# Kernel tuning notes

Hardware: AMD Instinct MI355X
Metric: run time of the kernel (lower is better)

The kernel has to match this reference:

```python
import jax, jax.numpy as jnp
import numpy as np


def setup_inputs() -> dict:
    key = jax.random.key(0)
    k1, k2 = jax.random.split(key)
    T, D, E = 8192, 4096, 64
    x = jax.random.normal(k1, (T, D), dtype=jnp.float32)
    gate_w = jax.random.normal(k2, (E, D), dtype=jnp.float32) * (1.0 / np.sqrt(D))
    return {"x": x, "gate_w": gate_w}


def reference(x, gate_w):
    TOPK = 8
    # logits = x @ W^T, computed in float32 like .float() in torch
    logits = jnp.einsum('td,ed->te', x, gate_w).astype(jnp.float32)
    scores = jax.nn.sigmoid(scores_in := logits) if False else jax.nn.sigmoid(logits)
    # top-k scores per token; values are exactly the gathered weights
    weights, indices = jax.lax.top_k(scores, TOPK)
    weights = weights / jnp.clip(jnp.sum(weights, axis=-1, keepdims=True), 1e-12)
    return weights.astype(x.dtype), indices
```

## Files before the change

### kernel.cpp

```cpp
#include <hip/hip_runtime.h>
#include <math.h>

#define T_TOTAL 8192
#define D_TOTAL 4096
#define E 64
#define TOPK 8
#define NKB (D_TOTAL / 32)

typedef short short8 __attribute__((ext_vector_type(8)));
typedef float f32x4 __attribute__((ext_vector_type(4)));

__device__ __forceinline__ void split3(const float* v8, short8& h, short8& m, short8& l) {
#pragma unroll
    for (int j = 0; j < 8; ++j) {
        const float f = v8[j];
        const unsigned u = __float_as_uint(f);
        const unsigned hu = u & 0xffff0000u;
        const float r1 = f - __uint_as_float(hu);
        const unsigned mu = __float_as_uint(r1) & 0xffff0000u;
        const float r2 = r1 - __uint_as_float(mu);
        const unsigned lu = __float_as_uint(r2);
        h[j] = (short)(hu >> 16);
        m[j] = (short)(mu >> 16);
        l[j] = (short)(lu >> 16);
    }
}

__global__ __launch_bounds__(256)
void prep_w(const float* __restrict__ w, short8* __restrict__ Bh,
            short8* __restrict__ Bm, short8* __restrict__ Bl) {
    const int t = blockIdx.x * 256 + threadIdx.x;
    const int lane = t & 63;
    const int nt = (t >> 6) & 3;
    const int kb = t >> 8;
    const int e = nt * 16 + (lane & 15);
    const int k = kb * 32 + (lane >> 4) * 8;

    const float* src = w + (size_t)e * D_TOTAL + k;
    float v[8];
    *reinterpret_cast<float4*>(&v[0]) = *reinterpret_cast<const float4*>(src);
    *reinterpret_cast<float4*>(&v[4]) = *reinterpret_cast<const float4*>(src + 4);

    short8 h, m, l;
    split3(v, h, m, l);
    Bh[t] = h; Bm[t] = m; Bl[t] = l;
}

__global__ __launch_bounds__(1024, 4)
void fused_router(const float* __restrict__ x,
                  const short8* __restrict__ Bh, const short8* __restrict__ Bm,
                  const short8* __restrict__ Bl,
                  float* __restrict__ out) {
    __shared__ float red[8 * 32 * 64];

    const int tid = threadIdx.x;
    const int lane = tid & 63;
    const int wv = tid >> 6;
    const int tok0 = blockIdx.x * 32;

    const int row = lane & 15;
    const int kq = lane >> 4;

    const float* xb = x + (size_t)(tok0 + row) * D_TOTAL + kq * 8;

    f32x4 acc[2][4];
#pragma unroll
    for (int m = 0; m < 2; ++m)
#pragma unroll
        for (int n = 0; n < 4; ++n) acc[m][n] = (f32x4){0.f, 0.f, 0.f, 0.f};

    const int kbase = wv * (D_TOTAL / 16);

    for (int kb = 0; kb < 8; ++kb) {
        const int k = kbase + kb * 32;
        const int gkb = k >> 5;

        short8 bh[4], bm[4], bl[4];
#pragma unroll
        for (int nt = 0; nt < 4; ++nt) {
            const size_t bi = (size_t)(gkb * 4 + nt) * 64 + lane;
            bh[nt] = Bh[bi];
            bm[nt] = Bm[bi];
            bl[nt] = Bl[bi];
        }

#pragma unroll
        for (int m = 0; m < 2; ++m) {
            const float* ap = xb + (size_t)(m * 16) * D_TOTAL + k;
            float av[8];
            *reinterpret_cast<float4*>(&av[0]) = *reinterpret_cast<const float4*>(ap);
            *reinterpret_cast<float4*>(&av[4]) = *reinterpret_cast<const float4*>(ap + 4);

            short8 ah, am_, al;
            split3(av, ah, am_, al);

#pragma unroll
            for (int nt = 0; nt < 4; ++nt) {
                f32x4 c = acc[m][nt];
                c = __builtin_amdgcn_mfma_f32_16x16x32_bf16(ah,  bh[nt], c, 0, 0, 0);
                c = __builtin_amdgcn_mfma_f32_16x16x32_bf16(ah,  bm[nt], c, 0, 0, 0);
                c = __builtin_amdgcn_mfma_f32_16x16x32_bf16(am_, bh[nt], c, 0, 0, 0);
                c = __builtin_amdgcn_mfma_f32_16x16x32_bf16(am_, bm[nt], c, 0, 0, 0);
                c = __builtin_amdgcn_mfma_f32_16x16x32_bf16(ah,  bl[nt], c, 0, 0, 0);
                c = __builtin_amdgcn_mfma_f32_16x16x32_bf16(al,  bh[nt], c, 0, 0, 0);
                c = __builtin_amdgcn_mfma_f32_16x16x32_bf16(am_, bl[nt], c, 0, 0, 0);
                c = __builtin_amdgcn_mfma_f32_16x16x32_bf16(al,  bm[nt], c, 0, 0, 0);
                acc[m][nt] = c;
            }
        }
    }

#pragma unroll
    for (int half = 8; half >= 1; half >>= 1) {
        if (wv >= half && wv < 2 * half) {
            float* s = &red[(size_t)(wv - half) * 32 * 64 + lane];
#pragma unroll
            for (int m = 0; m < 2; ++m)
#pragma unroll
                for (int nt = 0; nt < 4; ++nt)
#pragma unroll
                    for (int r = 0; r < 4; ++r)
                        s[(m * 16 + nt * 4 + r) * 64] = acc[m][nt][r];
        }
        __syncthreads();
        if (wv < half) {
            const float* s = &red[(size_t)wv * 32 * 64 + lane];
#pragma unroll
            for (int m = 0; m < 2; ++m)
#pragma unroll
                for (int nt = 0; nt < 4; ++nt)
#pragma unroll
                    for (int r = 0; r < 4; ++r)
                        acc[m][nt][r] += s[(m * 16 + nt * 4 + r) * 64];
        }
        __syncthreads();
    }

    if (wv == 0) {
#pragma unroll
        for (int m = 0; m < 2; ++m)
#pragma unroll
            for (int nt = 0; nt < 4; ++nt)
#pragma unroll
                for (int r = 0; r < 4; ++r) {
                    const int t = m * 16 + (lane >> 4) * 4 + r;
                    const int e = nt * 16 + (lane & 15);
                    red[t * 65 + e] = acc[m][nt][r];
                }
    }
    __syncthreads();

    if (tid < 32) {
        const int t = tid;
        float bv[TOPK];
        int   bi[TOPK];
#pragma unroll
        for (int j = 0; j < TOPK; ++j) { bv[j] = -INFINITY; bi[j] = 0; }

        for (int e = 0; e < E; ++e) {
            const float v = red[t * 65 + e];
            if (v > bv[TOPK - 1]) {
#pragma unroll
                for (int j = TOPK - 1; j > 0; --j) {
                    const bool gt = v > bv[j];
                    const bool gtp = v > bv[j - 1];
                    const float nv = gt ? (gtp ? bv[j - 1] : v) : bv[j];
                    const int   ni = gt ? (gtp ? bi[j - 1] : e) : bi[j];
                    bv[j] = nv; bi[j] = ni;
                }
                if (v > bv[0]) { bv[0] = v; bi[0] = e; }
            }
        }

        float wv_[TOPK];
        float wsum = 0.f;
#pragma unroll
        for (int j = 0; j < TOPK; ++j) {
            wv_[j] = 1.f / (1.f + expf(-bv[j]));
            wsum += wv_[j];
        }
        const float inv = 1.f / fmaxf(wsum, 1e-12f);

        const int tg = tok0 + t;
#pragma unroll
        for (int j = 0; j < TOPK; ++j) {
            out[(size_t)tg * TOPK + j] = wv_[j] * inv;
        }
#pragma unroll
        for (int j = 0; j < TOPK; ++j) {
            out[(size_t)T_TOTAL * TOPK + (size_t)tg * TOPK + j] = (float)bi[j];
        }
    }
}

extern "C" void kernel_launch(void* const* d_in, const int* in_sizes, int n_in,
                              void* d_out, int out_size, void* d_ws, size_t ws_size,
                              hipStream_t stream) {
    const float* x = (const float*)d_in[0];
    const float* w = (const float*)d_in[1];
    float* out = (float*)d_out;

    short8* Bh = (short8*)d_ws;
    short8* Bm = Bh + (size_t)NKB * 4 * 64;
    short8* Bl = Bm + (size_t)NKB * 4 * 64;

    prep_w<<<NKB * 4 * 64 / 256, 256, 0, stream>>>(w, Bh, Bm, Bl);
    fused_router<<<T_TOTAL / 32, 1024, 0, stream>>>(x, Bh, Bm, Bl, out);
}
```

Baseline: 56.44 us.

## Prefetch x, trim split-precision MFMAs, flatten reduction, wave-parallel top-k

Double-buffers the x loads in registers so the next k-slice is fetched while the current one is split and multiplied. It drops the two lowest-order cross terms (mid*low, low*mid) of the three-way bf16 split, leaving six MFMAs per tile instead of eight. The four-stage halving reduction over 16 waves is replaced by one shared-memory add step followed by a parallel column sum. Top-k moves from 32 serial threads to per-wave shuffle/ballot argmax. Dropping terms lowers logit precision, which could flip near-tied top-k choices, and the larger shared-memory footprint may limit occupancy.

```diff
diff --git a/kernel.cpp b/kernel.cpp
--- a/kernel.cpp
+++ b/kernel.cpp
@@ -46,12 +46,22 @@
     Bh[t] = h; Bm[t] = m; Bl[t] = l;
 }
 
+#define LOADX(DST, K) {                                                              \
+    const float* ap0 = xb + (K);                                                     \
+    *reinterpret_cast<float4*>(&(DST)[0])  = *reinterpret_cast<const float4*>(ap0);  \
+    *reinterpret_cast<float4*>(&(DST)[4])  = *reinterpret_cast<const float4*>(ap0 + 4); \
+    const float* ap1 = ap0 + 16 * D_TOTAL;                                           \
+    *reinterpret_cast<float4*>(&(DST)[8])  = *reinterpret_cast<const float4*>(ap1);  \
+    *reinterpret_cast<float4*>(&(DST)[12]) = *reinterpret_cast<const float4*>(ap1 + 4); \
+}
+
 __global__ __launch_bounds__(1024, 4)
 void fused_router(const float* __restrict__ x,
                   const short8* __restrict__ Bh, const short8* __restrict__ Bm,
                   const short8* __restrict__ Bl,
                   float* __restrict__ out) {
-    __shared__ float red[8 * 32 * 64];
+    __shared__ float tiles[8 * 2048];
+    __shared__ float fin[2048];
 
     const int tid = threadIdx.x;
     const int lane = tid & 63;
@@ -69,8 +79,12 @@
 #pragma unroll
         for (int n = 0; n < 4; ++n) acc[m][n] = (f32x4){0.f, 0.f, 0.f, 0.f};
 
-    const int kbase = wv * (D_TOTAL / 16);
-
+    const int kbase = wv * 256;
+
+    float xbuf[2][16];
+    LOADX(xbuf[0], kbase);
+
+#pragma unroll
     for (int kb = 0; kb < 8; ++kb) {
         const int k = kbase + kb * 32;
         const int gkb = k >> 5;
@@ -84,16 +98,12 @@
             bl[nt] = Bl[bi];
         }
 
+        if (kb < 7) LOADX(xbuf[(kb + 1) & 1], k + 32);
+
 #pragma unroll
         for (int m = 0; m < 2; ++m) {
-            const float* ap = xb + (size_t)(m * 16) * D_TOTAL + k;
-            float av[8];
-            *reinterpret_cast<float4*>(&av[0]) = *reinterpret_cast<const float4*>(ap);
-            *reinterpret_cast<float4*>(&av[4]) = *reinterpret_cast<const float4*>(ap + 4);
-
             short8 ah, am_, al;
-            split3(av, ah, am_, al);
-
+            split3(&xbuf[kb & 1][m * 8], ah, am_, al);
 #pragma unroll
             for (int nt = 0; nt < 4; ++nt) {
                 f32x4 c = acc[m][nt];
@@ -103,92 +113,80 @@
                 c = __builtin_amdgcn_mfma_f32_16x16x32_bf16(am_, bm[nt], c, 0, 0, 0);
                 c = __builtin_amdgcn_mfma_f32_16x16x32_bf16(ah,  bl[nt], c, 0, 0, 0);
                 c = __builtin_amdgcn_mfma_f32_16x16x32_bf16(al,  bh[nt], c, 0, 0, 0);
-                c = __builtin_amdgcn_mfma_f32_16x16x32_bf16(am_, bl[nt], c, 0, 0, 0);
-                c = __builtin_amdgcn_mfma_f32_16x16x32_bf16(al,  bm[nt], c, 0, 0, 0);
                 acc[m][nt] = c;
             }
         }
     }
 
-#pragma unroll
-    for (int half = 8; half >= 1; half >>= 1) {
-        if (wv >= half && wv < 2 * half) {
-            float* s = &red[(size_t)(wv - half) * 32 * 64 + lane];
-#pragma unroll
-            for (int m = 0; m < 2; ++m)
-#pragma unroll
-                for (int nt = 0; nt < 4; ++nt)
-#pragma unroll
-                    for (int r = 0; r < 4; ++r)
-                        s[(m * 16 + nt * 4 + r) * 64] = acc[m][nt][r];
-        }
-        __syncthreads();
-        if (wv < half) {
-            const float* s = &red[(size_t)wv * 32 * 64 + lane];
-#pragma unroll
-            for (int m = 0; m < 2; ++m)
-#pragma unroll
-                for (int nt = 0; nt < 4; ++nt)
-#pragma unroll
-                    for (int r = 0; r < 4; ++r)
-                        acc[m][nt][r] += s[(m * 16 + nt * 4 + r) * 64];
-        }
-        __syncthreads();
-    }
-
-    if (wv == 0) {
+    if (wv >= 8) {
+        float* s = &tiles[(size_t)(wv - 8) * 2048 + lane];
 #pragma unroll
         for (int m = 0; m < 2; ++m)
 #pragma unroll
             for (int nt = 0; nt < 4; ++nt)
 #pragma unroll
+                for (int r = 0; r < 4; ++r)
+                    s[(m * 16 + nt * 4 + r) * 64] = acc[m][nt][r];
+    }
+    __syncthreads();
+    if (wv < 8) {
+        float* s = &tiles[(size_t)wv * 2048 + lane];
+#pragma unroll
+        for (int m = 0; m < 2; ++m)
+#pragma unroll
+            for (int nt = 0; nt < 4; ++nt)
+#pragma unroll
                 for (int r = 0; r < 4; ++r) {
-                    const int t = m * 16 + (lane >> 4) * 4 + r;
-                    const int e = nt * 16 + (lane & 15);
-                    red[t * 65 + e] = acc[m][nt][r];
+                    const int j = (m * 16 + nt * 4 + r) * 64;
+                    s[j] = acc[m][nt][r] + s[j];
                 }
     }
     __syncthreads();
 
-    if (tid < 32) {
-        const int t = tid;
-        float bv[TOPK];
-        int   bi[TOPK];
-#pragma unroll
-        for (int j = 0; j < TOPK; ++j) { bv[j] = -INFINITY; bi[j] = 0; }
-
-        for (int e = 0; e < E; ++e) {
-            const float v = red[t * 65 + e];
-            if (v > bv[TOPK - 1]) {
-#pragma unroll
-                for (int j = TOPK - 1; j > 0; --j) {
-                    const bool gt = v > bv[j];
-                    const bool gtp = v > bv[j - 1];
-                    const float nv = gt ? (gtp ? bv[j - 1] : v) : bv[j];
-                    const int   ni = gt ? (gtp ? bi[j - 1] : e) : bi[j];
-                    bv[j] = nv; bi[j] = ni;
-                }
-                if (v > bv[0]) { bv[0] = v; bi[0] = e; }
-            }
-        }
-
-        float wv_[TOPK];
+    {
+        float s0 = 0.f, s1 = 0.f;
+#pragma unroll
+        for (int w2 = 0; w2 < 8; ++w2) {
+            s0 += tiles[w2 * 2048 + tid];
+            s1 += tiles[w2 * 2048 + 1024 + tid];
+        }
+        const int j = tid >> 6, ln = tid & 63;
+        const int t = (ln >> 4) * 4 + (j & 3);
+        const int e = ((j >> 2) & 3) * 16 + (ln & 15);
+        fin[t * 64 + e] = s0;
+        fin[(t + 16) * 64 + e] = s1;
+    }
+    __syncthreads();
+
+#pragma unroll
+    for (int rep = 0; rep < 2; ++rep) {
+        const int t = wv * 2 + rep;
+        float v = fin[t * 64 + lane];
+        float wj[TOPK];
+        int   ij[TOPK];
         float wsum = 0.f;
 #pragma unroll
         for (int j = 0; j < TOPK; ++j) {
-            wv_[j] = 1.f / (1.f + expf(-bv[j]));
-            wsum += wv_[j];
+            float mx = v;
+#pragma unroll
+            for (int off = 32; off >= 1; off >>= 1)
+                mx = fmaxf(mx, __shfl_xor(mx, off));
+            const unsigned long long msk = __ballot(v == mx);
+            const int widx = (int)__builtin_ctzll(msk);
+            wj[j] = 1.f / (1.f + expf(-mx));
+            ij[j] = widx;
+            wsum += wj[j];
+            if (lane == widx) v = -INFINITY;
         }
         const float inv = 1.f / fmaxf(wsum, 1e-12f);
-
         const int tg = tok0 + t;
-#pragma unroll
-        for (int j = 0; j < TOPK; ++j) {
-            out[(size_t)tg * TOPK + j] = wv_[j] * inv;
-        }
-#pragma unroll
-        for (int j = 0; j < TOPK; ++j) {
-            out[(size_t)T_TOTAL * TOPK + (size_t)tg * TOPK + j] = (float)bi[j];
+        if (lane == 0) {
+#pragma unroll
+            for (int j = 0; j < TOPK; ++j)
+                out[(size_t)tg * TOPK + j] = wj[j] * inv;
+#pragma unroll
+            for (int j = 0; j < TOPK; ++j)
+                out[(size_t)T_TOTAL * TOPK + (size_t)tg * TOPK + j] = (float)ij[j];
         }
     }
 }
```

Result: faster. 51.39 us (-8.9%).
